# Optimization experiments

Hardware: AMD Instinct MI355X
Metric: run time of the kernel (lower is better)

## Reference

```python
import jax, jax.numpy as jnp
import numpy as np
import math

EPS = 1e-5


def _layernorm(x, gamma, beta):
    mu = jnp.mean(x, axis=-1, keepdims=True)
    var = jnp.var(x, axis=-1, keepdims=True)
    return (x - mu) * jax.lax.rsqrt(var + EPS) * gamma + beta


def _quantum_head(x, theta_rx):
    # RX(x_i) then RX(theta_i) on wire i == RX(x_i + theta_i); product state,
    # CNOT ring is a Z-basis permutation => <Z_j> = prod_{i in S_j} cos(a_i)
    # with S_j = {0..j} for j>=1 (chain of CNOT(i,i+1)) and S_0 = {1..7}
    # (final CNOT(7,0) makes b0 = b1^...^b7).
    c = jnp.cos(x + theta_rx)                       # (B,S,8)
    cp = jnp.cumprod(c, axis=-1)                    # prefix products c0..cj
    z0 = jnp.prod(c[..., 1:], axis=-1, keepdims=True)
    return jnp.concatenate([z0, cp[..., 1:]], axis=-1)  # (B,S,8)


def _quantum_ffn(x, theta_ry):
    # RX(x_i) |0>, then RY(theta_i), measure Z: <Z_i> = cos(theta_i) * cos(x_i)
    return jnp.cos(theta_ry) * jnp.cos(x)


def setup_inputs() -> dict:
    key = jax.random.key(0)
    ks = jax.random.split(key, 6)
    B, S, E, F = 16, 2048, 8, 512
    return {
        'x': jax.random.normal(ks[0], (B, S, E), jnp.float32),
        'theta_rx': jax.random.normal(ks[1], (E,), jnp.float32),
        'w_out': jax.random.normal(ks[2], (E, E), jnp.float32) / math.sqrt(E),
        'theta_ry': jax.random.normal(ks[3], (E,), jnp.float32),
        'w1': jax.random.normal(ks[4], (F, E), jnp.float32) / math.sqrt(E),
        'b1': jnp.zeros((F,), jnp.float32),
        'w2': jax.random.normal(ks[5], (E, F), jnp.float32) / math.sqrt(F),
        'b2': jnp.zeros((E,), jnp.float32),
        'gamma1': jnp.ones((E,), jnp.float32),
        'beta1': jnp.zeros((E,), jnp.float32),
        'gamma2': jnp.ones((E,), jnp.float32),
        'beta2': jnp.zeros((E,), jnp.float32),
    }


def reference(x, theta_rx, w_out, theta_ry, w1, b1, w2, b2,
              gamma1, beta1, gamma2, beta2):
    B, S, E = x.shape
    H = 2
    D = E // H
    # --- quantum multi-head attention (shared head => q == k == v) ---
    z = _quantum_head(x, theta_rx)                       # (B,S,E)
    qh = z.reshape(B, S, H, D).transpose(0, 2, 1, 3)     # (B,H,S,D)
    scores = jnp.einsum('bhqd,bhkd->bhqk', qh, qh) / math.sqrt(D)
    attn = jax.nn.softmax(scores, axis=-1)
    out = jnp.einsum('bhqk,bhkd->bhqd', attn, qh)        # (B,H,S,D)
    out = out.transpose(0, 2, 1, 3).reshape(B, S, E)
    attn_out = out @ w_out.T                             # out_proj, no bias
    x1 = _layernorm(x + attn_out, gamma1, beta1)
    # --- quantum feed-forward ---
    zf = _quantum_ffn(x1, theta_ry)                      # (B,S,E)
    h = zf @ w1.T + b1                                   # (B,S,F)
    ffn_out = jax.nn.relu(h) @ w2.T + b2                 # (B,S,E)
    return _layernorm(x1 + ffn_out, gamma2, beta2)
```

## Files before the change

kernel.cpp:

```cpp
#include <hip/hip_runtime.h>
#include <math.h>
#include <utility>

#define NB 16
#define NS 2048
#define NE 8
#define NH 2
#define NF 512
#define DEG 6
#define NMONO 210
#define KPB 64
#define NCHUNK 32
#define PHI_LD 66
#define QPB 128
#define LNEPS 1e-5f
#define PART_STRIDE (5 * NMONO)

typedef float f32x2 __attribute__((ext_vector_type(2)));
typedef _Float16 h2 __attribute__((ext_vector_type(2)));

#if defined(__has_builtin)
# if __has_builtin(__builtin_amdgcn_fdot2)
#  define FDOT2(a,b,c) __builtin_amdgcn_fdot2((a),(b),(c),false)
# endif
#endif
#ifndef FDOT2
static __device__ __forceinline__ float fdot2_sw(h2 a, h2 b, float c) {
    return c + (float)a.x * (float)b.x + (float)a.y * (float)b.y;
}
# define FDOT2(a,b,c) fdot2_sw((a),(b),(c))
#endif

constexpr float ACOEF_C[7] = {0.99994459f, 2.00308514f, 2.00174650f,
                              1.30890404f, 0.65803033f, 0.31441604f, 0.10241921f};

constexpr int mono_e(int idx) {
    int i = 0;
    for (int e0 = 0; e0 <= DEG; ++e0)
        for (int e1 = 0; e1 <= DEG - e0; ++e1)
            for (int e2 = 0; e2 <= DEG - e0 - e1; ++e2)
                for (int e3 = 0; e3 <= DEG - e0 - e1 - e2; ++e3) {
                    if (i == idx) return (e0 << 12) | (e1 << 8) | (e2 << 4) | e3;
                    ++i;
                }
    return 0;
}
constexpr float mfact(int n) { float r = 1.f; for (int i = 2; i <= n; ++i) r *= (float)i; return r; }
constexpr float mono_c(int idx) {
    const int E = mono_e(idx);
    const int e0 = E >> 12, e1 = (E >> 8) & 15, e2 = (E >> 4) & 15, e3 = E & 15;
    const int d = e0 + e1 + e2 + e3;
    return ACOEF_C[d] * (mfact(d) / (mfact(e0) * mfact(e1) * mfact(e2) * mfact(e3)));
}

template <int BEG, class F, int... Is>
__device__ __forceinline__ void sf_impl(F f, std::integer_sequence<int, Is...>) {
    (f(std::integral_constant<int, BEG + Is>{}), ...);
}
template <int BEG, int END, class F>
__device__ __forceinline__ void static_for(F f) {
    sf_impl<BEG>(f, std::make_integer_sequence<int, END - BEG>{});
}

template <int BEG, int END>
__device__ __forceinline__ void phi_body(_Float16* __restrict__ Phi, int lane,
                                         const float (&pw0)[7], const float (&pw1)[7],
                                         const float (&pw2)[7], const float (&pw3)[7]) {
    static_for<BEG, END>([&](auto Ic) {
        constexpr int idx = Ic.value;
        constexpr int E = mono_e(idx);
        constexpr float C = mono_c(idx);
        const float v = C * (pw0[E >> 12] * pw1[(E >> 8) & 15]) *
                            (pw2[(E >> 4) & 15] * pw3[E & 15]);
        Phi[idx * PHI_LD + lane] = (_Float16)v;
    });
}

__global__ __launch_bounds__(256, 4)
void k1_moments(const float* __restrict__ x, const float* __restrict__ theta_rx,
                float* __restrict__ ws) {
    __shared__ _Float16 Phi[NMONO * PHI_LD];
    __shared__ __align__(16) _Float16 kvh[KPB / 2][8];
    __shared__ float th_s[8];

    const int t = threadIdx.x, bid = blockIdx.x;
    const int kc = bid & 31, h = (bid >> 5) & 1, b = bid >> 6;

    if (t < 8) th_s[t] = theta_rx[t];
    __syncthreads();

    const int lane = t & 63, wq = t >> 6;
    {
        const float* xr = x + ((size_t)b * NS + kc * KPB + lane) * NE;
        const float4 v0 = *reinterpret_cast<const float4*>(xr);
        const float4 v1 = *reinterpret_cast<const float4*>(xr + 4);
        const float c0 = __cosf(v0.x + th_s[0]), c1 = __cosf(v0.y + th_s[1]);
        const float c2 = __cosf(v0.z + th_s[2]), c3 = __cosf(v0.w + th_s[3]);
        const float c4 = __cosf(v1.x + th_s[4]), c5 = __cosf(v1.y + th_s[5]);
        const float c6 = __cosf(v1.z + th_s[6]), c7 = __cosf(v1.w + th_s[7]);
        const float p1 = c0*c1, p2 = p1*c2, p3 = p2*c3, p4 = p3*c4;
        const float p5 = p4*c5, p6 = p5*c6, p7 = p6*c7;
        float k0, k1v, k2v, k3v;
        if (h == 0) {
            const float s6 = c7*c6, s5 = s6*c5, s4 = s5*c4, s3 = s4*c3, s2 = s3*c2;
            k0 = s2*c1; k1v = p1; k2v = p2; k3v = p3;
        } else {
            k0 = p4; k1v = p5; k2v = p6; k3v = p7;
        }
        if (t < 64) {
            const int j = t >> 1, par = t & 1;
            kvh[j][0 + par] = (_Float16)k0;  kvh[j][2 + par] = (_Float16)k1v;
            kvh[j][4 + par] = (_Float16)k2v; kvh[j][6 + par] = (_Float16)k3v;
        }
        float pw0[7], pw1[7], pw2[7], pw3[7];
        pw0[0] = pw1[0] = pw2[0] = pw3[0] = 1.f;
        #pragma unroll
        for (int i = 1; i <= DEG; ++i) {
            pw0[i] = pw0[i-1] * k0;  pw1[i] = pw1[i-1] * k1v;
            pw2[i] = pw2[i-1] * k2v; pw3[i] = pw3[i-1] * k3v;
        }
        switch (wq) {
            case 0: phi_body<0,   53 >(Phi, lane, pw0, pw1, pw2, pw3); break;
            case 1: phi_body<53,  106>(Phi, lane, pw0, pw1, pw2, pw3); break;
            case 2: phi_body<106, 159>(Phi, lane, pw0, pw1, pw2, pw3); break;
            default: phi_body<159, 210>(Phi, lane, pw0, pw1, pw2, pw3); break;
        }
    }
    __syncthreads();

    if (t < NMONO) {
        const h2 one2 = {(_Float16)1.f, (_Float16)1.f};
        float a0 = 0.f, a1 = 0.f, a2 = 0.f, a3 = 0.f, a4 = 0.f;
        #pragma unroll 8
        for (int j = 0; j < KPB / 2; ++j) {
            const h2 phi2 = *reinterpret_cast<const h2*>(&Phi[t * PHI_LD + 2 * j]);
            const float4 kv4 = *reinterpret_cast<const float4*>(&kvh[j][0]);
            const h2 kA = __builtin_bit_cast(h2, kv4.x);
            const h2 kB = __builtin_bit_cast(h2, kv4.y);
            const h2 kC = __builtin_bit_cast(h2, kv4.z);
            const h2 kD = __builtin_bit_cast(h2, kv4.w);
            a0 = FDOT2(phi2, kA, a0);
            a1 = FDOT2(phi2, kB, a1);
            a2 = FDOT2(phi2, kC, a2);
            a3 = FDOT2(phi2, kD, a3);
            a4 = FDOT2(phi2, one2, a4);
        }
        float* dst = ws + (size_t)bid * PART_STRIDE;
        dst[0 * NMONO + t] = a0;
        dst[1 * NMONO + t] = a1;
        dst[2 * NMONO + t] = a2;
        dst[3 * NMONO + t] = a3;
        dst[4 * NMONO + t] = a4;
    }
}

template <int BEG, int END>
__device__ __forceinline__ void p2_body2(const float4* __restrict__ Mn,
                                         const float* __restrict__ Md, int base,
                                         const float (&pwA)[4][7], const float (&pwB)[4][7],
                                         f32x2& a01A, f32x2& a23A, float& adA,
                                         f32x2& a01B, f32x2& a23B, float& adB) {
    static_for<BEG, END>([&](auto Ic) {
        constexpr int idx = Ic.value;
        constexpr int E = mono_e(idx);
        constexpr int e0 = E >> 12, e1 = (E >> 8) & 15, e2 = (E >> 4) & 15, e3 = E & 15;
        const float4 mv = Mn[base + idx];
        const float  md = Md[base + idx];
        const f32x2 m01 = {mv.x, mv.y}, m23 = {mv.z, mv.w};
        const float PA = (pwA[0][e0] * pwA[1][e1]) * (pwA[2][e2] * pwA[3][e3]);
        const float PB = (pwB[0][e0] * pwB[1][e1]) * (pwB[2][e2] * pwB[3][e3]);
        a01A += PA * m01;  a23A += PA * m23;  adA += PA * md;
        a01B += PB * m01;  a23B += PB * m23;  adB += PB * md;
    });
}

__global__ __launch_bounds__(1024)
void k2_main(const float* __restrict__ x, const float* __restrict__ theta_rx,
             const float* __restrict__ w_out, const float* __restrict__ theta_ry,
             const float* __restrict__ w1, const float* __restrict__ b1,
             const float* __restrict__ w2, const float* __restrict__ b2,
             const float* __restrict__ g1, const float* __restrict__ be1,
             const float* __restrict__ g2, const float* __restrict__ be2,
             const float* __restrict__ ws, float* __restrict__ out) {
    __shared__ float4 Mn_lds[2 * NMONO];
    __shared__ float  Md_lds[2 * NMONO];
    __shared__ float  z_c[8][QPB];
    __shared__ float  x1_c[8][QPB];
    __shared__ float  zf_c[8][QPB];
    __shared__ float  attn_c[8][QPB];
    __shared__ float  part_a[4][256][5];
    __shared__ float  part_f[8][QPB][9];
    __shared__ float  w1_s[NF][NE];
    __shared__ float  w2t_s[NF][NE];
    __shared__ float  b1_s[NF];
    __shared__ float  wout_s[NE][NE];
    __shared__ float  th_s[8], cry_s[8], g1_s[8], be1_s[8], g2_s[8], be2_s[8], b2_s[8];

    const int t = threadIdx.x, bid = blockIdx.x;
    const int b = bid >> 4, qc = bid & 15;

    float (*scr)[5] = (float(*)[5])&part_f[0][0][0];

    for (int i = t; i < NF * NE; i += 1024) {
        ((float*)w1_s)[i] = w1[i];
        const int e = i >> 9, f = i & (NF - 1);
        w2t_s[f][e] = w2[i];
    }
    if (t < NF) b1_s[t] = b1[t];
    if (t < NE * NE) ((float*)wout_s)[t] = w_out[t];
    if (t < 8) {
        th_s[t]  = theta_rx[t];
        cry_s[t] = __cosf(theta_ry[t]);
        g1_s[t]  = g1[t];  be1_s[t] = be1[t];
        g2_s[t]  = g2[t];  be2_s[t] = be2[t];
        b2_s[t]  = b2[t];
    }
    if (t < 840) {
        const int half = t / 420;
        const int a2 = t - half * 420;
        const int h = (a2 >= NMONO) ? 1 : 0;
        const int a = a2 - h * NMONO;
        const float* src = ws + (size_t)((b * 2 + h) * NCHUNK + half * 16) * PART_STRIDE;
        float s0 = 0.f, s1 = 0.f, s2 = 0.f, s3 = 0.f, s4 = 0.f;
        #pragma unroll 4
        for (int kc = 0; kc < 16; ++kc) {
            const float* p = src + (size_t)kc * PART_STRIDE;
            s0 += p[0 * NMONO + a]; s1 += p[1 * NMONO + a];
            s2 += p[2 * NMONO + a]; s3 += p[3 * NMONO + a];
            s4 += p[4 * NMONO + a];
        }
        float* d = scr[t];
        d[0] = s0; d[1] = s1; d[2] = s2; d[3] = s3; d[4] = s4;
    }
    if (t >= 896) {
        const int r = t - 896;
        const float* xr = x + ((size_t)b * NS + qc * QPB + r) * NE;
        const float4 v0 = *reinterpret_cast<const float4*>(xr);
        const float4 v1 = *reinterpret_cast<const float4*>(xr + 4);
        const float4 ta = *reinterpret_cast<const float4*>(theta_rx);
        const float4 tb = *reinterpret_cast<const float4*>(theta_rx + 4);
        const float c0 = __cosf(v0.x + ta.x), c1 = __cosf(v0.y + ta.y);
        const float c2 = __cosf(v0.z + ta.z), c3 = __cosf(v0.w + ta.w);
        const float c4 = __cosf(v1.x + tb.x), c5 = __cosf(v1.y + tb.y);
        const float c6 = __cosf(v1.z + tb.z), c7 = __cosf(v1.w + tb.w);
        const float p1 = c0*c1, p2 = p1*c2, p3 = p2*c3, p4 = p3*c4;
        const float p5 = p4*c5, p6 = p5*c6, p7 = p6*c7;
        const float s6 = c7*c6, s5 = s6*c5, s4 = s5*c4, s3 = s4*c3, s2 = s3*c2;
        z_c[0][r] = s2*c1; z_c[1][r] = p1; z_c[2][r] = p2; z_c[3][r] = p3;
        z_c[4][r] = p4;    z_c[5][r] = p5; z_c[6][r] = p6; z_c[7][r] = p7;
    }
    __syncthreads();

    if (t < 2 * NMONO) {
        const float* pa = scr[t];
        const float* pb = scr[t + 420];
        Mn_lds[t] = make_float4(pa[0] + pb[0], pa[1] + pb[1],
                                pa[2] + pb[2], pa[3] + pb[3]);
        Md_lds[t] = pa[4] + pb[4];
    }
    __syncthreads();

    if (t < 512) {
        const int w = t >> 6, l = t & 63;
        const int g = w >> 1, h = w & 1;
        const int rA = l, rB = l + 64;
        float pwA[4][7], pwB[4][7];
        #pragma unroll
        for (int d = 0; d < 4; ++d) {
            const float uA = z_c[h*4+d][rA] * 0.25f;
            const float uB = z_c[h*4+d][rB] * 0.25f;
            pwA[d][0] = 1.f; pwB[d][0] = 1.f;
            #pragma unroll
            for (int i = 1; i <= DEG; ++i) {
                pwA[d][i] = pwA[d][i-1] * uA;
                pwB[d][i] = pwB[d][i-1] * uB;
            }
        }
        f32x2 a01A = {0.f,0.f}, a23A = {0.f,0.f}, a01B = {0.f,0.f}, a23B = {0.f,0.f};
        float adA = 0.f, adB = 0.f;
        const int base = h * NMONO;
        switch (g) {
            case 0: p2_body2<0,   53 >(Mn_lds, Md_lds, base, pwA, pwB, a01A, a23A, adA, a01B, a23B, adB); break;
            case 1: p2_body2<53,  106>(Mn_lds, Md_lds, base, pwA, pwB, a01A, a23A, adA, a01B, a23B, adB); break;
            case 2: p2_body2<106, 159>(Mn_lds, Md_lds, base, pwA, pwB, a01A, a23A, adA, a01B, a23B, adB); break;
            default: p2_body2<159, 210>(Mn_lds, Md_lds, base, pwA, pwB, a01A, a23A, adA, a01B, a23B, adB); break;
        }
        float* pa = &part_a[g][h * 128 + rA][0];
        pa[0] = a01A.x; pa[1] = a01A.y; pa[2] = a23A.x; pa[3] = a23A.y; pa[4] = adA;
        float* pb = &part_a[g][h * 128 + rB][0];
        pb[0] = a01B.x; pb[1] = a01B.y; pb[2] = a23B.x; pb[3] = a23B.y; pb[4] = adB;
    }
    __syncthreads();

    if (t < 256) {
        const int h = t >> 7, r = t & 127;
        float n0 = 0.f, n1 = 0.f, n2 = 0.f, n3 = 0.f, dd = 0.f;
        #pragma unroll
        for (int g = 0; g < 4; ++g) {
            const float* pa = &part_a[g][t][0];
            n0 += pa[0]; n1 += pa[1]; n2 += pa[2]; n3 += pa[3]; dd += pa[4];
        }
        const float inv = 1.0f / dd;
        attn_c[h*4+0][r] = n0 * inv; attn_c[h*4+1][r] = n1 * inv;
        attn_c[h*4+2][r] = n2 * inv; attn_c[h*4+3][r] = n3 * inv;
    }
    __syncthreads();

    if (t < QPB) {
        float av[NE];
        #pragma unroll
        for (int e = 0; e < NE; ++e) av[e] = attn_c[e][t];
        float y[NE];
        #pragma unroll
        for (int e = 0; e < NE; ++e) {
            float acc = 0.f;
            #pragma unroll
            for (int k = 0; k < NE; ++k) acc += av[k] * wout_s[e][k];
            y[e] = acc;
        }
        const float* xr = x + ((size_t)b * NS + qc * QPB + t) * NE;
        const float4 xv0 = *reinterpret_cast<const float4*>(xr);
        const float4 xv1 = *reinterpret_cast<const float4*>(xr + 4);
        float t1[NE];
        t1[0] = xv0.x + y[0]; t1[1] = xv0.y + y[1]; t1[2] = xv0.z + y[2]; t1[3] = xv0.w + y[3];
        t1[4] = xv1.x + y[4]; t1[5] = xv1.y + y[5]; t1[6] = xv1.z + y[6]; t1[7] = xv1.w + y[7];
        float mu = 0.f;
        #pragma unroll
        for (int e = 0; e < NE; ++e) mu += t1[e];
        mu *= 0.125f;
        float var = 0.f;
        #pragma unroll
        for (int e = 0; e < NE; ++e) { const float d = t1[e] - mu; var += d * d; }
        var *= 0.125f;
        const float inv1 = rsqrtf(var + LNEPS);
        #pragma unroll
        for (int e = 0; e < NE; ++e) {
            const float x1e = (t1[e] - mu) * inv1 * g1_s[e] + be1_s[e];
            x1_c[e][t] = x1e;
            zf_c[e][t] = cry_s[e] * __cosf(x1e);
        }
    }
    __syncthreads();

    if (t < 256) {
        const int fs = t >> 5;
        const int rr = t & 31;
        f32x2 zf01[4], zf23[4], zf45[4], zf67[4];
        #pragma unroll
        for (int k = 0; k < 4; ++k) {
            const int row = rr + 32 * k;
            zf01[k] = (f32x2){zf_c[0][row], zf_c[1][row]};
            zf23[k] = (f32x2){zf_c[2][row], zf_c[3][row]};
            zf45[k] = (f32x2){zf_c[4][row], zf_c[5][row]};
            zf67[k] = (f32x2){zf_c[6][row], zf_c[7][row]};
        }
        f32x2 a01[4] = {}, a23[4] = {}, a45[4] = {}, a67[4] = {};
        #pragma unroll 4
        for (int i = 0; i < 64; ++i) {
            const int f = fs * 64 + i;
            const float4 wa = *reinterpret_cast<const float4*>(&w1_s[f][0]);
            const float4 wb = *reinterpret_cast<const float4*>(&w1_s[f][4]);
            const float bb = b1_s[f];
            const float4 ua = *reinterpret_cast<const float4*>(&w2t_s[f][0]);
            const float4 ub = *reinterpret_cast<const float4*>(&w2t_s[f][4]);
            const f32x2 wa01 = {wa.x, wa.y}, wa23 = {wa.z, wa.w};
            const f32x2 wb45 = {wb.x, wb.y}, wb67 = {wb.z, wb.w};
            const f32x2 ua01 = {ua.x, ua.y}, ua23 = {ua.z, ua.w};
            const f32x2 ub45 = {ub.x, ub.y}, ub67 = {ub.z, ub.w};
            #pragma unroll
            for (int k = 0; k < 4; ++k) {
                const f32x2 ha = zf01[k] * wa01 + zf23[k] * wa23;
                const f32x2 hb = zf45[k] * wb45 + zf67[k] * wb67;
                float hv = bb + ha.x + ha.y + hb.x + hb.y;
                hv = fmaxf(hv, 0.f);
                a01[k] += hv * ua01;  a23[k] += hv * ua23;
                a45[k] += hv * ub45;  a67[k] += hv * ub67;
            }
        }
        #pragma unroll
        for (int k = 0; k < 4; ++k) {
            const int row = rr + 32 * k;
            float* pf = &part_f[fs][row][0];
            pf[0] = a01[k].x; pf[1] = a01[k].y; pf[2] = a23[k].x; pf[3] = a23[k].y;
            pf[4] = a45[k].x; pf[5] = a45[k].y; pf[6] = a67[k].x; pf[7] = a67[k].y;
        }
    }
    __syncthreads();

    {
        const int e = t >> 7, r = t & 127;
        float s = 0.f;
        #pragma unroll
        for (int fs = 0; fs < 8; ++fs) s += part_f[fs][r][e];
        zf_c[e][r] = x1_c[e][r] + s + b2_s[e];
    }
    __syncthreads();

    if (t < QPB) {
        float t2[NE];
        #pragma unroll
        for (int e = 0; e < NE; ++e) t2[e] = zf_c[e][t];
        float mu = 0.f;
        #pragma unroll
        for (int e = 0; e < NE; ++e) mu += t2[e];
        mu *= 0.125f;
        float var = 0.f;
        #pragma unroll
        for (int e = 0; e < NE; ++e) { const float d = t2[e] - mu; var += d * d; }
        var *= 0.125f;
        const float inv2 = rsqrtf(var + LNEPS);
        float o[NE];
        #pragma unroll
        for (int e = 0; e < NE; ++e) o[e] = (t2[e] - mu) * inv2 * g2_s[e] + be2_s[e];
        float4* o4 = reinterpret_cast<float4*>(out + ((size_t)b * NS + qc * QPB + t) * NE);
        o4[0] = make_float4(o[0], o[1], o[2], o[3]);
        o4[1] = make_float4(o[4], o[5], o[6], o[7]);
    }
}

extern "C" void kernel_launch(void* const* d_in, const int* in_sizes, int n_in,
                              void* d_out, int out_size, void* d_ws, size_t ws_size,
                              hipStream_t stream) {
    const float* x        = (const float*)d_in[0];
    const float* theta_rx = (const float*)d_in[1];
    const float* w_out    = (const float*)d_in[2];
    const float* theta_ry = (const float*)d_in[3];
    const float* w1       = (const float*)d_in[4];
    const float* b1       = (const float*)d_in[5];
    const float* w2       = (const float*)d_in[6];
    const float* b2       = (const float*)d_in[7];
    const float* g1       = (const float*)d_in[8];
    const float* be1      = (const float*)d_in[9];
    const float* g2       = (const float*)d_in[10];
    const float* be2      = (const float*)d_in[11];
    float* out = (float*)d_out;
    float* ws  = (float*)d_ws;

    k1_moments<<<dim3(NB * NH * NCHUNK), dim3(256), 0, stream>>>(x, theta_rx, ws);
    k2_main<<<dim3(NB * (NS / QPB)), dim3(1024), 0, stream>>>(
        x, theta_rx, w_out, theta_ry, w1, b1, w2, b2, g1, be1, g2, be2, ws, out);
}
```

Before: 35.80 us.

## Spread FFN over all 1024 threads with shuffle reduction and fuse reduction phases

The FFN stage now runs on all 1024 threads: eight lanes per row each take a strided slice of the 512 hidden units, and their partial outputs are summed with wave shuffles instead of an LDS partial buffer. This removes the part_f buffer and two __syncthreads barriers. The attention partial-sum reduction is folded into the out-projection step, which drops another barrier and the attn_c buffer. In exchange the w1 and w2 rows are no longer reused across four rows per thread, so each thread does more LDS reads per FLOP. Each thread also writes a single scalar output instead of two float4 stores.

```diff
diff --git a/kernel.cpp b/kernel.cpp
--- a/kernel.cpp
+++ b/kernel.cpp
@@ -187,19 +187,17 @@
     __shared__ float  z_c[8][QPB];
     __shared__ float  x1_c[8][QPB];
     __shared__ float  zf_c[8][QPB];
-    __shared__ float  attn_c[8][QPB];
     __shared__ float  part_a[4][256][5];
-    __shared__ float  part_f[8][QPB][9];
     __shared__ float  w1_s[NF][NE];
     __shared__ float  w2t_s[NF][NE];
     __shared__ float  b1_s[NF];
     __shared__ float  wout_s[NE][NE];
-    __shared__ float  th_s[8], cry_s[8], g1_s[8], be1_s[8], g2_s[8], be2_s[8], b2_s[8];
+    __shared__ float  cry_s[8], g1_s[8], be1_s[8], g2_s[8], be2_s[8], b2_s[8];
 
     const int t = threadIdx.x, bid = blockIdx.x;
     const int b = bid >> 4, qc = bid & 15;
 
-    float (*scr)[5] = (float(*)[5])&part_f[0][0][0];
+    float (*scr)[5] = (float(*)[5])&part_a[0][0][0];
 
     for (int i = t; i < NF * NE; i += 1024) {
         ((float*)w1_s)[i] = w1[i];
@@ -209,7 +207,6 @@
     if (t < NF) b1_s[t] = b1[t];
     if (t < NE * NE) ((float*)wout_s)[t] = w_out[t];
     if (t < 8) {
-        th_s[t]  = theta_rx[t];
         cry_s[t] = __cosf(theta_ry[t]);
         g1_s[t]  = g1[t];  be1_s[t] = be1[t];
         g2_s[t]  = g2[t];  be2_s[t] = be2[t];
@@ -292,24 +289,20 @@
     }
     __syncthreads();
 
-    if (t < 256) {
-        const int h = t >> 7, r = t & 127;
-        float n0 = 0.f, n1 = 0.f, n2 = 0.f, n3 = 0.f, dd = 0.f;
-        #pragma unroll
-        for (int g = 0; g < 4; ++g) {
-            const float* pa = &part_a[g][t][0];
-            n0 += pa[0]; n1 += pa[1]; n2 += pa[2]; n3 += pa[3]; dd += pa[4];
-        }
-        const float inv = 1.0f / dd;
-        attn_c[h*4+0][r] = n0 * inv; attn_c[h*4+1][r] = n1 * inv;
-        attn_c[h*4+2][r] = n2 * inv; attn_c[h*4+3][r] = n3 * inv;
-    }
-    __syncthreads();
-
     if (t < QPB) {
         float av[NE];
         #pragma unroll
-        for (int e = 0; e < NE; ++e) av[e] = attn_c[e][t];
+        for (int h = 0; h < 2; ++h) {
+            float n0 = 0.f, n1 = 0.f, n2 = 0.f, n3 = 0.f, dd = 0.f;
+            #pragma unroll
+            for (int g = 0; g < 4; ++g) {
+                const float* pa = &part_a[g][h * 128 + t][0];
+                n0 += pa[0]; n1 += pa[1]; n2 += pa[2]; n3 += pa[3]; dd += pa[4];
+            }
+            const float inv = 1.0f / dd;
+            av[h*4+0] = n0 * inv; av[h*4+1] = n1 * inv;
+            av[h*4+2] = n2 * inv; av[h*4+3] = n3 * inv;
+        }
         float y[NE];
         #pragma unroll
         for (int e = 0; e < NE; ++e) {
@@ -342,64 +335,36 @@
     }
     __syncthreads();
 
-    if (t < 256) {
-        const int fs = t >> 5;
-        const int rr = t & 31;
-        f32x2 zf01[4], zf23[4], zf45[4], zf67[4];
-        #pragma unroll
-        for (int k = 0; k < 4; ++k) {
-            const int row = rr + 32 * k;
-            zf01[k] = (f32x2){zf_c[0][row], zf_c[1][row]};
-            zf23[k] = (f32x2){zf_c[2][row], zf_c[3][row]};
-            zf45[k] = (f32x2){zf_c[4][row], zf_c[5][row]};
-            zf67[k] = (f32x2){zf_c[6][row], zf_c[7][row]};
-        }
-        f32x2 a01[4] = {}, a23[4] = {}, a45[4] = {}, a67[4] = {};
-        #pragma unroll 4
+    {
+        const int r = t >> 3, sub = t & 7;
+        float zf[NE];
+        #pragma unroll
+        for (int e = 0; e < NE; ++e) zf[e] = zf_c[e][r];
+        f32x2 a01 = {0.f,0.f}, a23 = {0.f,0.f}, a45 = {0.f,0.f}, a67 = {0.f,0.f};
+        #pragma unroll 8
         for (int i = 0; i < 64; ++i) {
-            const int f = fs * 64 + i;
+            const int f = sub + (i << 3);
             const float4 wa = *reinterpret_cast<const float4*>(&w1_s[f][0]);
             const float4 wb = *reinterpret_cast<const float4*>(&w1_s[f][4]);
-            const float bb = b1_s[f];
+            float hv = b1_s[f] + zf[0]*wa.x + zf[1]*wa.y + zf[2]*wa.z + zf[3]*wa.w
+                               + zf[4]*wb.x + zf[5]*wb.y + zf[6]*wb.z + zf[7]*wb.w;
+            hv = fmaxf(hv, 0.f);
             const float4 ua = *reinterpret_cast<const float4*>(&w2t_s[f][0]);
             const float4 ub = *reinterpret_cast<const float4*>(&w2t_s[f][4]);
-            const f32x2 wa01 = {wa.x, wa.y}, wa23 = {wa.z, wa.w};
-            const f32x2 wb45 = {wb.x, wb.y}, wb67 = {wb.z, wb.w};
-            const f32x2 ua01 = {ua.x, ua.y}, ua23 = {ua.z, ua.w};
-            const f32x2 ub45 = {ub.x, ub.y}, ub67 = {ub.z, ub.w};
+            a01 += hv * (f32x2){ua.x, ua.y};
+            a23 += hv * (f32x2){ua.z, ua.w};
+            a45 += hv * (f32x2){ub.x, ub.y};
+            a67 += hv * (f32x2){ub.z, ub.w};
+        }
+        float acc[NE] = {a01.x, a01.y, a23.x, a23.y, a45.x, a45.y, a67.x, a67.y};
+        #pragma unroll
+        for (int m = 1; m < 8; m <<= 1) {
             #pragma unroll
-            for (int k = 0; k < 4; ++k) {
-                const f32x2 ha = zf01[k] * wa01 + zf23[k] * wa23;
-                const f32x2 hb = zf45[k] * wb45 + zf67[k] * wb67;
-                float hv = bb + ha.x + ha.y + hb.x + hb.y;
-                hv = fmaxf(hv, 0.f);
-                a01[k] += hv * ua01;  a23[k] += hv * ua23;
-                a45[k] += hv * ub45;  a67[k] += hv * ub67;
-            }
-        }
-        #pragma unroll
-        for (int k = 0; k < 4; ++k) {
-            const int row = rr + 32 * k;
-            float* pf = &part_f[fs][row][0];
-            pf[0] = a01[k].x; pf[1] = a01[k].y; pf[2] = a23[k].x; pf[3] = a23[k].y;
-            pf[4] = a45[k].x; pf[5] = a45[k].y; pf[6] = a67[k].x; pf[7] = a67[k].y;
-        }
-    }
-    __syncthreads();
-
-    {
-        const int e = t >> 7, r = t & 127;
-        float s = 0.f;
-        #pragma unroll
-        for (int fs = 0; fs < 8; ++fs) s += part_f[fs][r][e];
-        zf_c[e][r] = x1_c[e][r] + s + b2_s[e];
-    }
-    __syncthreads();
-
-    if (t < QPB) {
+            for (int e = 0; e < NE; ++e) acc[e] += __shfl_xor(acc[e], m, 64);
+        }
         float t2[NE];
         #pragma unroll
-        for (int e = 0; e < NE; ++e) t2[e] = zf_c[e][t];
+        for (int e = 0; e < NE; ++e) t2[e] = x1_c[e][r] + acc[e] + b2_s[e];
         float mu = 0.f;
         #pragma unroll
         for (int e = 0; e < NE; ++e) mu += t2[e];
@@ -409,12 +374,8 @@
         for (int e = 0; e < NE; ++e) { const float d = t2[e] - mu; var += d * d; }
         var *= 0.125f;
         const float inv2 = rsqrtf(var + LNEPS);
-        float o[NE];
-        #pragma unroll
-        for (int e = 0; e < NE; ++e) o[e] = (t2[e] - mu) * inv2 * g2_s[e] + be2_s[e];
-        float4* o4 = reinterpret_cast<float4*>(out + ((size_t)b * NS + qc * QPB + t) * NE);
-        o4[0] = make_float4(o[0], o[1], o[2], o[3]);
-        o4[1] = make_float4(o[4], o[5], o[6], o[7]);
+        out[((size_t)b * NS + qc * QPB + r) * NE + sub] =
+            (t2[sub] - mu) * inv2 * g2_s[sub] + be2_s[sub];
     }
 }
 
```

Result: slower. 60.52 us (+69.0%).
